# Performance work log

Measured on AMD Instinct MI355X. Metric: run time of the kernel, lower is better.

The kernel has to match this reference:

```python
import jax, jax.numpy as jnp
import numpy as np

SPATIAL_SHAPES = [(100, 152), (50, 76), (25, 38), (13, 19)]
D_MODEL = 256
N_HEADS = 8
N_LEVELS = 4
N_POINTS = 4
D_FFN = 1024
D_HEAD = D_MODEL // N_HEADS
EPS = 1e-5


def layernorm(x, g, b):
    mu = jnp.mean(x, axis=-1, keepdims=True)
    var = jnp.var(x, axis=-1, keepdims=True)
    return (x - mu) * jax.lax.rsqrt(var + EPS) * g + b


def bilinear_sample(value_l, H, W, locs):
    # value_l: (N, H*W, nH, dH); locs: (N, Lq, nH, P, 2) normalized to [0,1]
    # Matches torch grid_sample(align_corners=False, padding_mode='zeros') with grid=2*loc-1.
    N, Lq = locs.shape[0], locs.shape[1]
    x = locs[..., 0] * W - 0.5  # (N, Lq, nH, P) pixel coords
    y = locs[..., 1] * H - 0.5
    x0 = jnp.floor(x)
    y0 = jnp.floor(y)
    fx = x - x0
    fy = y - y0
    x0 = x0.astype(jnp.int32)
    y0 = y0.astype(jnp.int32)
    out = jnp.zeros((N, Lq, N_POINTS, N_HEADS, D_HEAD), value_l.dtype)
    for dy in (0, 1):
        for dx in (0, 1):
            xi = x0 + dx
            yi = y0 + dy
            w = (fx if dx else 1.0 - fx) * (fy if dy else 1.0 - fy)
            valid = (xi >= 0) & (xi < W) & (yi >= 0) & (yi < H)
            idx = jnp.clip(yi, 0, H - 1) * W + jnp.clip(xi, 0, W - 1)  # (N, Lq, nH, P)
            idx = idx.transpose(0, 1, 3, 2).reshape(N, Lq * N_POINTS, N_HEADS, 1)
            g = jnp.take_along_axis(value_l, idx, axis=1)  # (N, Lq*P, nH, dH)
            g = g.reshape(N, Lq, N_POINTS, N_HEADS, D_HEAD)
            wv = jnp.where(valid, w, 0.0).transpose(0, 1, 3, 2)[..., None]  # (N, Lq, P, nH, 1)
            out = out + g * wv
    return out  # (N, Lq, P, nH, dH)


def msdeform_attn(query, value_in, ref_points,
                  w_value, b_value, w_off, b_off, w_attn, b_attn, w_out, b_out):
    N, Lq, _ = query.shape
    value = (value_in @ w_value + b_value).reshape(N, -1, N_HEADS, D_HEAD)
    off = (query @ w_off + b_off).reshape(N, Lq, N_HEADS, N_LEVELS, N_POINTS, 2)
    attn = (query @ w_attn + b_attn).reshape(N, Lq, N_HEADS, N_LEVELS * N_POINTS)
    attn = jax.nn.softmax(attn, axis=-1).reshape(N, Lq, N_HEADS, N_LEVELS, N_POINTS)
    # offset normalizer is (W, H) per level
    norm = jnp.array([[w, h] for (h, w) in SPATIAL_SHAPES], dtype=query.dtype)  # (L, 2)
    locs = ref_points[:, :, None, :, None, :] + off / norm[None, None, None, :, None, :]
    out = jnp.zeros((N, Lq, N_HEADS, D_HEAD), query.dtype)
    start = 0
    for l, (H, W) in enumerate(SPATIAL_SHAPES):
        v_l = value[:, start:start + H * W]
        s = bilinear_sample(v_l, H, W, locs[:, :, :, l])  # (N, Lq, P, nH, dH)
        out = out + jnp.einsum('nqhp,nqphd->nqhd', attn[:, :, :, l], s)
        start += H * W
    out = out.reshape(N, Lq, D_MODEL)
    return out @ w_out + b_out


def setup_inputs() -> dict:
    key = jax.random.key(0)
    ks = jax.random.split(key, 20)
    B = 2
    Lq = sum(h * w for h, w in SPATIAL_SHAPES)  # 20197
    scale = 0.02
    inp = {
        'src': jax.random.normal(ks[0], (B, Lq, D_MODEL), jnp.float32),
        'pos': jax.random.normal(ks[1], (B, Lq, D_MODEL), jnp.float32),
        'reference_points': jax.random.uniform(ks[2], (B, Lq, N_LEVELS, 2), jnp.float32),
        'spatial_shapes': jnp.array(SPATIAL_SHAPES, dtype=jnp.int32),
        'level_start_index': jnp.array(np.cumsum([0] + [h * w for h, w in SPATIAL_SHAPES[:-1]]), dtype=jnp.int32),
        'w_value': jax.random.normal(ks[3], (D_MODEL, D_MODEL), jnp.float32) * scale,
        'b_value': jnp.zeros((D_MODEL,), jnp.float32),
        'w_off': jax.random.normal(ks[4], (D_MODEL, N_HEADS * N_LEVELS * N_POINTS * 2), jnp.float32) * scale,
        'b_off': jax.random.normal(ks[5], (N_HEADS * N_LEVELS * N_POINTS * 2,), jnp.float32) * scale,
        'w_attn': jax.random.normal(ks[6], (D_MODEL, N_HEADS * N_LEVELS * N_POINTS), jnp.float32) * scale,
        'b_attn': jnp.zeros((N_HEADS * N_LEVELS * N_POINTS,), jnp.float32),
        'w_out': jax.random.normal(ks[7], (D_MODEL, D_MODEL), jnp.float32) * scale,
        'b_out': jnp.zeros((D_MODEL,), jnp.float32),
        'g1': jnp.ones((D_MODEL,), jnp.float32),
        'beta1': jnp.zeros((D_MODEL,), jnp.float32),
        'w1': jax.random.normal(ks[8], (D_MODEL, D_FFN), jnp.float32) * scale,
        'b1': jnp.zeros((D_FFN,), jnp.float32),
        'w2': jax.random.normal(ks[9], (D_FFN, D_MODEL), jnp.float32) * scale,
        'b2': jnp.zeros((D_MODEL,), jnp.float32),
        'g2': jnp.ones((D_MODEL,), jnp.float32),
        'beta2': jnp.zeros((D_MODEL,), jnp.float32),
    }
    return inp


def reference(src, pos, reference_points, spatial_shapes, level_start_index,
              w_value, b_value, w_off, b_off, w_attn, b_attn, w_out, b_out,
              g1, beta1, w1, b1, w2, b2, g2, beta2):
    query = src + pos
    src2 = msdeform_attn(query, src, reference_points,
                         w_value, b_value, w_off, b_off, w_attn, b_attn, w_out, b_out)
    src = layernorm(src + src2, g1, beta1)
    h = jax.nn.relu(src @ w1 + b1)
    src = layernorm(src + h @ w2 + b2, g2, beta2)
    return src
```

## Files before the change

kernel.cpp:

```cpp
#include <hip/hip_runtime.h>

#define LQ   20197
#define MTOT 40394

typedef _Float16 f16;
typedef _Float16 f16x8 __attribute__((ext_vector_type(8)));
typedef _Float16 f16x4 __attribute__((ext_vector_type(4)));
typedef _Float16 f16x2 __attribute__((ext_vector_type(2)));
typedef float    f32x4 __attribute__((ext_vector_type(4)));

#define OFF_B4 1507328ull
#define OFF_B1 42870784ull
#define OFF_B2 63552512ull
#define OFF_B3 84234240ull
#define OFF_B5 104915968ull
#define OFF_B6 125597696ull
#define OFF_B7 166961152ull

#define WT_V    0
#define WT_OFF  65536
#define WT_ATTN 131072
#define WT_OUT  163840
#define WT_W1   229376
#define WT_W2   491520
#define WT_TOTAL 753664
#define WCONV_TOTAL (WT_TOTAL + 384)
#define PREP_TOTAL (MTOT * 64)
#define FUSED_TOTAL (WCONV_TOTAL + PREP_TOTAL)

__device__ __forceinline__ void gload_lds16(const f16* g, f16* l) {
    __builtin_amdgcn_global_load_lds(
        (const __attribute__((address_space(1))) unsigned int*)g,
        (__attribute__((address_space(3))) unsigned int*)l,
        16, 0, 0);
}

__global__ __launch_bounds__(256) void k_wconv_prep(
    const float* __restrict__ wv, const float* __restrict__ woff,
    const float* __restrict__ wattn, const float* __restrict__ wout,
    const float* __restrict__ w1, const float* __restrict__ w2,
    const float* __restrict__ boff, const float* __restrict__ battn,
    f16* __restrict__ dst, float* __restrict__ biasoa,
    const float* __restrict__ srcf, const float* __restrict__ posf,
    f16* __restrict__ srch, f16* __restrict__ qh)
{
    int gid = blockIdx.x * 256 + threadIdx.x;
    if (gid >= FUSED_TOTAL) return;
    if (gid >= WCONV_TOTAL) {
        const int i = gid - WCONV_TOTAL;
        float4 s = ((const float4*)srcf)[i];
        float4 p = ((const float4*)posf)[i];
        f16x4 hs = { (f16)s.x, (f16)s.y, (f16)s.z, (f16)s.w };
        f16x4 hq = { (f16)(s.x + p.x), (f16)(s.y + p.y), (f16)(s.z + p.z), (f16)(s.w + p.w) };
        ((f16x4*)srch)[i] = hs;
        ((f16x4*)qh)[i]   = hq;
        return;
    }
    if (gid >= WT_TOTAL) {
        int i = gid - WT_TOTAL;
        biasoa[i] = (i < 256) ? boff[i] : battn[i - 256];
        return;
    }
    const float* src; int Kd, Nd, base;
    if      (gid < 65536)  { src = wv;    Kd = 256;  Nd = 256;  base = 0; }
    else if (gid < 131072) { src = woff;  Kd = 256;  Nd = 256;  base = 65536; }
    else if (gid < 163840) { src = wattn; Kd = 256;  Nd = 128;  base = 131072; }
    else if (gid < 229376) { src = wout;  Kd = 256;  Nd = 256;  base = 163840; }
    else if (gid < 491520) { src = w1;    Kd = 256;  Nd = 1024; base = 229376; }
    else                   { src = w2;    Kd = 1024; Nd = 256;  base = 491520; }
    int loc = gid - base;
    int n = loc % Nd, k = loc / Nd;
    dst[base + n * Kd + k] = (f16)src[k * Nd + n];
}

template<bool RELU, int OUTM>
__global__ __launch_bounds__(256) void k_gemm128(
    const f16* __restrict__ A, const f16* __restrict__ Bt,
    const float* __restrict__ bias, void* __restrict__ Cout,
    int M, int N, int K)
{
    __shared__ __align__(16) char pool[34816];
    f16* const sm = (f16*)pool;

    const int NBn = N >> 7;
    const int MBn = (M + 127) >> 7;
    const int tiles = MBn * NBn;
    const int q = gridDim.x >> 3;
    const int bid = blockIdx.x;
    const int swz = (bid & 7) * q + (bid >> 3);
    if (swz >= tiles) return;
    const int m0 = (swz / NBn) << 7;
    const int n0 = (swz % NBn) << 7;

    const int t = threadIdx.x, wid = t >> 6, lane = t & 63;

    const int c0 = wid, c1 = wid + 4;
    const int sr = lane >> 2, sk = (lane & 3) * 8;
    const int ra0 = min(m0 + c0 * 16 + sr, M - 1);
    const int ra1 = min(m0 + c1 * 16 + sr, M - 1);
    const f16* pa0 = A + (size_t)ra0 * K + sk;
    const f16* pa1 = A + (size_t)ra1 * K + sk;
    const f16* pb0 = Bt + (size_t)(n0 + c0 * 16 + sr) * K + sk;
    const f16* pb1 = Bt + (size_t)(n0 + c1 * 16 + sr) * K + sk;
    const int lo0 = c0 * 512, lo1 = c1 * 512;

    const int wr = wid >> 1, wc = wid & 1;
    const int fr = lane & 15, kb = (lane >> 4) * 8;

    f32x4 acc[4][4] = {};
    const int NT = K >> 5;

    gload_lds16(pa0, sm + lo0);
    gload_lds16(pa1, sm + lo1);
    gload_lds16(pb0, sm + 4096 + lo0);
    gload_lds16(pb1, sm + 4096 + lo1);
    __syncthreads();

    for (int tt = 0; tt < NT; ++tt) {
        const int cur = (tt & 1) << 13, nxt = cur ^ 8192;
        if (tt + 1 < NT) {
            const int k0 = (tt + 1) << 5;
            gload_lds16(pa0 + k0, sm + nxt + lo0);
            gload_lds16(pa1 + k0, sm + nxt + lo1);
            gload_lds16(pb0 + k0, sm + nxt + 4096 + lo0);
            gload_lds16(pb1 + k0, sm + nxt + 4096 + lo1);
        }
        f16x8 af[4], bf[4];
#pragma unroll
        for (int i = 0; i < 4; ++i)
            af[i] = *(const f16x8*)&sm[cur + (wr * 64 + i * 16 + fr) * 32 + kb];
#pragma unroll
        for (int i = 0; i < 4; ++i)
            bf[i] = *(const f16x8*)&sm[cur + 4096 + (wc * 64 + i * 16 + fr) * 32 + kb];
#pragma unroll
        for (int mi = 0; mi < 4; ++mi)
#pragma unroll
            for (int ni = 0; ni < 4; ++ni)
                acc[mi][ni] = __builtin_amdgcn_mfma_f32_16x16x32_f16(af[mi], bf[ni], acc[mi][ni], 0, 0, 0);
        __syncthreads();
    }

    const int r4 = (lane >> 4) * 4;
#pragma unroll
    for (int ni = 0; ni < 4; ++ni) {
        const int lcol = wc * 64 + ni * 16 + fr;
        const float bv = bias[n0 + lcol];
#pragma unroll
        for (int mi = 0; mi < 4; ++mi) {
#pragma unroll
            for (int j = 0; j < 4; ++j) {
                float v = acc[mi][ni][j] + bv;
                if (RELU) v = fmaxf(v, 0.f);
                sm[(wr * 64 + mi * 16 + r4 + j) * 136 + lcol] = (f16)v;
            }
        }
    }
    __syncthreads();

    if (OUTM == 1) {
        const int rr = t >> 4, cc = (t & 15) * 8;
#pragma unroll
        for (int pass = 0; pass < 8; ++pass) {
            const int r = pass * 16 + rr;
            const int row = m0 + r;
            if (row < M) {
                f16x8 v = *(const f16x8*)&sm[r * 136 + cc];
                *(f16x8*)&((f16*)Cout)[(size_t)row * N + n0 + cc] = v;
            }
        }
    } else {
        const int cbl = t >> 6, rr = (t & 63) >> 2, cc = (t & 3) * 8;
        const size_t cb = (size_t)((n0 >> 5) + cbl);
#pragma unroll
        for (int pass = 0; pass < 8; ++pass) {
            const int r = pass * 16 + rr;
            const int row = m0 + r;
            if (row < M) {
                f16x8 v = *(const f16x8*)&sm[r * 136 + cbl * 32 + cc];
                *(f16x8*)&((f16*)Cout)[(cb * M + row) * 32 + cc] = v;
            }
        }
    }
}

__global__ __launch_bounds__(256) void k_sample(
    const f16* __restrict__ oa, const f16* __restrict__ valueT,
    const float* __restrict__ ref, f16* __restrict__ samp)
{
    __shared__ uint2 s_g[64][17];
    __shared__ f16x4 s_w[64][17];
    const int head = blockIdx.x & 7;
    const int tok0 = (blockIdx.x >> 3) * 64;
    const int t = threadIdx.x;

#pragma unroll
    for (int it = 0; it < 4; ++it) {
        const int tl = it * 16 + (t >> 4);
        const int lp = t & 15, l = lp >> 2;
        const int tok = tok0 + tl;
        if (tok < MTOT) {
            const size_t row = (size_t)tok * 384;
            float logit = (float)oa[row + 256 + head * 16 + lp];
            float mx = logit;
#pragma unroll
            for (int m = 1; m < 16; m <<= 1) mx = fmaxf(mx, __shfl_xor(mx, m));
            float e = __expf(logit - mx);
            float sum = e;
#pragma unroll
            for (int m = 1; m < 16; m <<= 1) sum += __shfl_xor(sum, m);
            const float aw = e / sum;

            const float fW = (l == 0) ? 152.f : (l == 1) ? 76.f : (l == 2) ? 38.f : 19.f;
            const float fH = (l == 0) ? 100.f : (l == 1) ? 50.f : (l == 2) ? 25.f : 13.f;
            const int   W  = (l == 0) ? 152 : (l == 1) ? 76 : (l == 2) ? 38 : 19;
            const int   H  = (l == 0) ? 100 : (l == 1) ? 50 : (l == 2) ? 25 : 13;
            const int   st = (l == 0) ? 0 : (l == 1) ? 15200 : (l == 2) ? 19000 : 19950;

            const f16x2 ov = *(const f16x2*)&oa[row + head * 32 + lp * 2];
            const float2 rxy = *(const float2*)&ref[(size_t)tok * 8 + l * 2];
            const float x = rxy.x * fW + (float)ov.x - 0.5f;
            const float y = rxy.y * fH + (float)ov.y - 0.5f;
            const float xf = floorf(x), yf = floorf(y);
            const float fx = x - xf, fy = y - yf;
            const int x0 = (int)xf, y0 = (int)yf;

            const bool vx0 = (x0 >= 0) && (x0 < W);
            const bool vx1 = (x0 >= -1) && (x0 < W - 1);
            const bool vy0 = (y0 >= 0) && (y0 < H);
            const bool vy1 = (y0 >= -1) && (y0 < H - 1);
            const int x0c = min(max(x0, 0), W - 1), x1c = min(max(x0 + 1, 0), W - 1);
            const int y0c = min(max(y0, 0), H - 1), y1c = min(max(y0 + 1, 0), H - 1);

            const int n = (tok >= LQ) ? 1 : 0;
            const unsigned int b00 = (unsigned int)(n * LQ + st + y0c * W + x0c) << 6;
            const unsigned int dx6 = (unsigned int)(x1c - x0c) << 6;
            const unsigned int dy6 = (unsigned int)((y1c - y0c) * W) << 6;
            s_g[tl][lp] = make_uint2(b00, dx6 | (dy6 << 16));

            const f16 w00 = (f16)((vx0 && vy0) ? (1.f - fx) * (1.f - fy) * aw : 0.f);
            const f16 w01 = (f16)((vx1 && vy0) ? fx * (1.f - fy) * aw : 0.f);
            const f16 w10 = (f16)((vx0 && vy1) ? (1.f - fx) * fy * aw : 0.f);
            const f16 w11 = (f16)((vx1 && vy1) ? fx * fy * aw : 0.f);
            f16x4 wv = { w00, w01, w10, w11 };
            s_w[tl][lp] = wv;
        }
    }
    __syncthreads();

    const int tl = t >> 2, l4 = t & 3;
    const int tok = tok0 + tl;
    if (tok >= MTOT) return;
    const unsigned int lb = (unsigned int)l4 * 16u;
    const char* vbase = (const char*)valueT + (size_t)head * (MTOT * 64ull);

    f16x2 a0 = {}, a1 = {}, a2 = {}, a3 = {};
#pragma unroll 4
    for (int p = 0; p < 16; ++p) {
        const uint2 g  = s_g[tl][p];
        const f16x4 wv = s_w[tl][p];
        const unsigned int a00 = g.x + lb;
        const unsigned int dx6 = g.y & 0xFFFFu;
        const unsigned int dy6 = g.y >> 16;
        const f16x8 v00 = *(const f16x8*)(vbase + a00);
        const f16x8 v01 = *(const f16x8*)(vbase + (a00 + dx6));
        const f16x8 v10 = *(const f16x8*)(vbase + (a00 + dy6));
        const f16x8 v11 = *(const f16x8*)(vbase + (a00 + dy6 + dx6));
        const f16x2 w0 = { wv[0], wv[0] }, w1 = { wv[1], wv[1] };
        const f16x2 w2 = { wv[2], wv[2] }, w3 = { wv[3], wv[3] };
        const f16x2* p0 = (const f16x2*)&v00;
        const f16x2* p1 = (const f16x2*)&v01;
        const f16x2* p2 = (const f16x2*)&v10;
        const f16x2* p3 = (const f16x2*)&v11;
        a0 = a0 + p0[0] * w0; a1 = a1 + p0[1] * w0;
        a2 = a2 + p0[2] * w0; a3 = a3 + p0[3] * w0;
        a0 = a0 + p1[0] * w1; a1 = a1 + p1[1] * w1;
        a2 = a2 + p1[2] * w1; a3 = a3 + p1[3] * w1;
        a0 = a0 + p2[0] * w2; a1 = a1 + p2[1] * w2;
        a2 = a2 + p2[2] * w2; a3 = a3 + p2[3] * w2;
        a0 = a0 + p3[0] * w3; a1 = a1 + p3[1] * w3;
        a2 = a2 + p3[2] * w3; a3 = a3 + p3[3] * w3;
    }
    f16x8 o = { a0.x, a0.y, a1.x, a1.y, a2.x, a2.y, a3.x, a3.y };
    *(f16x8*)&samp[(size_t)tok * 256 + head * 32 + l4 * 8] = o;
}

template<int OUTF16>
__global__ __launch_bounds__(256) void k_lnh(
    const f16* __restrict__ xa, const f16* __restrict__ xb,
    const float* __restrict__ g, const float* __restrict__ be,
    void* __restrict__ y, int M)
{
    const int row = blockIdx.x * 4 + (threadIdx.x >> 6);
    const int lane = threadIdx.x & 63;
    if (row >= M) return;
    const size_t o = (size_t)row * 256 + lane * 4;
    f16x4 a = *(const f16x4*)(xa + o);
    f16x4 b = *(const f16x4*)(xb + o);
    float x0 = (float)a.x + (float)b.x, x1 = (float)a.y + (float)b.y;
    float x2 = (float)a.z + (float)b.z, x3 = (float)a.w + (float)b.w;
    float s  = x0 + x1 + x2 + x3;
    float ss = x0*x0 + x1*x1 + x2*x2 + x3*x3;
#pragma unroll
    for (int m = 1; m < 64; m <<= 1) { s += __shfl_xor(s, m); ss += __shfl_xor(ss, m); }
    const float mean = s * (1.f / 256.f);
    const float var  = ss * (1.f / 256.f) - mean * mean;
    const float rstd = rsqrtf(var + 1e-5f);
    float4 gv = *(const float4*)(g + lane * 4);
    float4 bv = *(const float4*)(be + lane * 4);
    const float y0 = (x0 - mean) * rstd * gv.x + bv.x;
    const float y1 = (x1 - mean) * rstd * gv.y + bv.y;
    const float y2 = (x2 - mean) * rstd * gv.z + bv.z;
    const float y3 = (x3 - mean) * rstd * gv.w + bv.w;
    if (OUTF16) {
        f16x4 hv = { (f16)y0, (f16)y1, (f16)y2, (f16)y3 };
        *(f16x4*)((f16*)y + o) = hv;
    } else {
        float4 yo = { y0, y1, y2, y3 };
        *(float4*)((float*)y + o) = yo;
    }
}

extern "C" void kernel_launch(void* const* d_in, const int* in_sizes, int n_in,
                              void* d_out, int out_size, void* d_ws, size_t ws_size,
                              hipStream_t stream) {
    const float* src   = (const float*)d_in[0];
    const float* pos   = (const float*)d_in[1];
    const float* ref   = (const float*)d_in[2];
    const float* w_value = (const float*)d_in[5];
    const float* b_value = (const float*)d_in[6];
    const float* w_off   = (const float*)d_in[7];
    const float* b_off   = (const float*)d_in[8];
    const float* w_attn  = (const float*)d_in[9];
    const float* b_attn  = (const float*)d_in[10];
    const float* w_out   = (const float*)d_in[11];
    const float* b_out   = (const float*)d_in[12];
    const float* g1    = (const float*)d_in[13];
    const float* beta1 = (const float*)d_in[14];
    const float* w1    = (const float*)d_in[15];
    const float* b1    = (const float*)d_in[16];
    const float* w2    = (const float*)d_in[17];
    const float* b2    = (const float*)d_in[18];
    const float* g2    = (const float*)d_in[19];
    const float* beta2 = (const float*)d_in[20];

    char* ws = (char*)d_ws;
    f16*   wT      = (f16*)(ws + 0);
    f16*   oa      = (f16*)(ws + OFF_B4);
    f16*   y2h     = (f16*)(ws + OFF_B4);
    f16*   srch    = (f16*)(ws + OFF_B1);
    f16*   qh      = (f16*)(ws + OFF_B2);
    f16*   x1h     = (f16*)(ws + OFF_B2);
    f16*   valueT  = (f16*)(ws + OFF_B3);
    f16*   hh      = (f16*)(ws + OFF_B3);
    float* biasoa  = (float*)(ws + OFF_B5);
    f16*   src2h   = (f16*)(ws + OFF_B6);
    f16*   samph   = (f16*)(ws + OFF_B7);
    float* outp    = (float*)d_out;

    const int M = MTOT;
    const int MB = (M + 127) / 128;
    auto grid8 = [&](int nb) { return ((MB * nb) + 7) & ~7; };

    k_wconv_prep<<<(FUSED_TOTAL + 255) / 256, 256, 0, stream>>>(
        w_value, w_off, w_attn, w_out, w1, w2, b_off, b_attn, wT, biasoa,
        src, pos, srch, qh);

    k_gemm128<false, 2><<<grid8(2), 256, 0, stream>>>(srch, wT + WT_V, b_value, valueT, M, 256, 256);
    k_gemm128<false, 1><<<grid8(3), 256, 0, stream>>>(qh, wT + WT_OFF, biasoa, oa, M, 384, 256);
    {
        const int nchunk = (MTOT + 63) / 64;
        k_sample<<<dim3(nchunk * 8), 256, 0, stream>>>(oa, valueT, ref, samph);
    }
    k_gemm128<false, 1><<<grid8(2), 256, 0, stream>>>(samph, wT + WT_OUT, b_out, src2h, M, 256, 256);
    k_lnh<1><<<(M + 3) / 4, 256, 0, stream>>>(srch, src2h, g1, beta1, x1h, M);
    k_gemm128<true, 1><<<grid8(8), 256, 0, stream>>>(x1h, wT + WT_W1, b1, hh, M, 1024, 256);
    k_gemm128<false, 1><<<grid8(2), 256, 0, stream>>>(hh, wT + WT_W2, b2, y2h, M, 256, 1024);
    k_lnh<0><<<(M + 3) / 4, 256, 0, stream>>>(x1h, y2h, g2, beta2, outp, M);

    (void)in_sizes; (void)n_in; (void)out_size; (void)ws_size;
}
```

Baseline: 220.4 us.

## Split bilinear corner pairs across threads in deformable sampling kernel

```diff
diff --git a/kernel.cpp b/kernel.cpp
--- a/kernel.cpp
+++ b/kernel.cpp
@@ -187,14 +187,14 @@
     const f16* __restrict__ oa, const f16* __restrict__ valueT,
     const float* __restrict__ ref, f16* __restrict__ samp)
 {
-    __shared__ uint2 s_g[64][17];
-    __shared__ f16x4 s_w[64][17];
+    __shared__ int2  s_g[32][17];
+    __shared__ f16x4 s_w[32][17];
     const int head = blockIdx.x & 7;
-    const int tok0 = (blockIdx.x >> 3) * 64;
+    const int tok0 = (blockIdx.x >> 3) * 32;
     const int t = threadIdx.x;
 
 #pragma unroll
-    for (int it = 0; it < 4; ++it) {
+    for (int it = 0; it < 2; ++it) {
         const int tl = it * 16 + (t >> 4);
         const int lp = t & 15, l = lp >> 2;
         const int tok = tok0 + tl;
@@ -228,14 +228,13 @@
             const bool vx1 = (x0 >= -1) && (x0 < W - 1);
             const bool vy0 = (y0 >= 0) && (y0 < H);
             const bool vy1 = (y0 >= -1) && (y0 < H - 1);
-            const int x0c = min(max(x0, 0), W - 1), x1c = min(max(x0 + 1, 0), W - 1);
             const int y0c = min(max(y0, 0), H - 1), y1c = min(max(y0 + 1, 0), H - 1);
+            const int bx  = min(max(x0, -1), W - 1);
 
             const int n = (tok >= LQ) ? 1 : 0;
-            const unsigned int b00 = (unsigned int)(n * LQ + st + y0c * W + x0c) << 6;
-            const unsigned int dx6 = (unsigned int)(x1c - x0c) << 6;
-            const unsigned int dy6 = (unsigned int)((y1c - y0c) * W) << 6;
-            s_g[tl][lp] = make_uint2(b00, dx6 | (dy6 << 16));
+            const int b00 = (n * LQ + st + y0c * W + bx) << 6;
+            const int dy6 = ((y1c - y0c) * W) << 6;
+            s_g[tl][lp] = make_int2(b00, dy6);
 
             const f16 w00 = (f16)((vx0 && vy0) ? (1.f - fx) * (1.f - fy) * aw : 0.f);
             const f16 w01 = (f16)((vx1 && vy0) ? fx * (1.f - fy) * aw : 0.f);
@@ -247,41 +246,44 @@
     }
     __syncthreads();
 
-    const int tl = t >> 2, l4 = t & 3;
+    const int tl = t >> 3;
+    const int g3 = t & 7;
+    const int xc = g3 >> 2;
+    const int l4 = g3 & 3;
     const int tok = tok0 + tl;
     if (tok >= MTOT) return;
-    const unsigned int lb = (unsigned int)l4 * 16u;
+    const int lb = g3 * 16;
     const char* vbase = (const char*)valueT + (size_t)head * (MTOT * 64ull);
 
     f16x2 a0 = {}, a1 = {}, a2 = {}, a3 = {};
 #pragma unroll 4
     for (int p = 0; p < 16; ++p) {
-        const uint2 g  = s_g[tl][p];
+        const int2  g  = s_g[tl][p];
         const f16x4 wv = s_w[tl][p];
-        const unsigned int a00 = g.x + lb;
-        const unsigned int dx6 = g.y & 0xFFFFu;
-        const unsigned int dy6 = g.y >> 16;
-        const f16x8 v00 = *(const f16x8*)(vbase + a00);
-        const f16x8 v01 = *(const f16x8*)(vbase + (a00 + dx6));
-        const f16x8 v10 = *(const f16x8*)(vbase + (a00 + dy6));
-        const f16x8 v11 = *(const f16x8*)(vbase + (a00 + dy6 + dx6));
-        const f16x2 w0 = { wv[0], wv[0] }, w1 = { wv[1], wv[1] };
-        const f16x2 w2 = { wv[2], wv[2] }, w3 = { wv[3], wv[3] };
-        const f16x2* p0 = (const f16x2*)&v00;
-        const f16x2* p1 = (const f16x2*)&v01;
-        const f16x2* p2 = (const f16x2*)&v10;
-        const f16x2* p3 = (const f16x2*)&v11;
-        a0 = a0 + p0[0] * w0; a1 = a1 + p0[1] * w0;
-        a2 = a2 + p0[2] * w0; a3 = a3 + p0[3] * w0;
-        a0 = a0 + p1[0] * w1; a1 = a1 + p1[1] * w1;
-        a2 = a2 + p1[2] * w1; a3 = a3 + p1[3] * w1;
-        a0 = a0 + p2[0] * w2; a1 = a1 + p2[1] * w2;
-        a2 = a2 + p2[2] * w2; a3 = a3 + p2[3] * w2;
-        a0 = a0 + p3[0] * w3; a1 = a1 + p3[1] * w3;
-        a2 = a2 + p3[2] * w3; a3 = a3 + p3[3] * w3;
-    }
-    f16x8 o = { a0.x, a0.y, a1.x, a1.y, a2.x, a2.y, a3.x, a3.y };
-    *(f16x8*)&samp[(size_t)tok * 256 + head * 32 + l4 * 8] = o;
+        const char* base = vbase + (g.x + lb);
+        const f16x8 vA = *(const f16x8*)(base);
+        const f16x8 vB = *(const f16x8*)(base + g.y);
+        const f16 wa = xc ? wv[1] : wv[0];
+        const f16 wb = xc ? wv[3] : wv[2];
+        const f16x2 wA = { wa, wa }, wB = { wb, wb };
+        const f16x2* pA = (const f16x2*)&vA;
+        const f16x2* pB = (const f16x2*)&vB;
+        a0 = a0 + pA[0] * wA; a1 = a1 + pA[1] * wA;
+        a2 = a2 + pA[2] * wA; a3 = a3 + pA[3] * wA;
+        a0 = a0 + pB[0] * wB; a1 = a1 + pB[1] * wB;
+        a2 = a2 + pB[2] * wB; a3 = a3 + pB[3] * wB;
+    }
+
+    union { f16x2 h; int i; } u0, u1, u2, u3;
+    u0.h = a0; u1.h = a1; u2.h = a2; u3.h = a3;
+    union { int i; f16x2 h; } r0, r1, r2, r3;
+    r0.i = __shfl_xor(u0.i, 4); r1.i = __shfl_xor(u1.i, 4);
+    r2.i = __shfl_xor(u2.i, 4); r3.i = __shfl_xor(u3.i, 4);
+    a0 = a0 + r0.h; a1 = a1 + r1.h; a2 = a2 + r2.h; a3 = a3 + r3.h;
+
+    f16x4 o = xc ? (f16x4){ a2.x, a2.y, a3.x, a3.y }
+                 : (f16x4){ a0.x, a0.y, a1.x, a1.y };
+    *(f16x4*)&samp[(size_t)tok * 256 + head * 32 + l4 * 8 + xc * 4] = o;
 }
 
 template<int OUTF16>
@@ -352,7 +354,7 @@
     f16*   x1h     = (f16*)(ws + OFF_B2);
     f16*   valueT  = (f16*)(ws + OFF_B3);
     f16*   hh      = (f16*)(ws + OFF_B3);
-    float* biasoa  = (float*)(ws + OFF_B5);
+    float* biasoa  = (float*)(ws + OFF_B5 + 128);
     f16*   src2h   = (f16*)(ws + OFF_B6);
     f16*   samph   = (f16*)(ws + OFF_B7);
     float* outp    = (float*)d_out;
@@ -368,7 +370,7 @@
     k_gemm128<false, 2><<<grid8(2), 256, 0, stream>>>(srch, wT + WT_V, b_value, valueT, M, 256, 256);
     k_gemm128<false, 1><<<grid8(3), 256, 0, stream>>>(qh, wT + WT_OFF, biasoa, oa, M, 384, 256);
     {
-        const int nchunk = (MTOT + 63) / 64;
+        const int nchunk = (MTOT + 31) / 32;
         k_sample<<<dim3(nchunk * 8), 256, 0, stream>>>(oa, valueT, ref, samph);
     }
     k_gemm128<false, 1><<<grid8(2), 256, 0, stream>>>(samph, wT + WT_OUT, b_out, src2h, M, 256, 256);
```

Result: faster. 211.3 us (-4.2%).
